# Kernel tuning notes

Hardware: AMD Instinct MI355X
Metric: run time of the kernel (lower is better)

Reference implementation:

```python
import jax, jax.numpy as jnp
import numpy as np

_INF = -1e30
EPS = 1e-8


def _masked_max(v, mask, axis, keepdims=False):
    return jnp.max(jnp.where(mask == 0, _INF, v), axis=axis, keepdims=keepdims)


def _masked_mean(v, mask, axis, keepdims=False):
    s = jnp.sum(jnp.where(mask == 0, 0.0, v), axis=axis, keepdims=keepdims)
    cnt = jnp.sum(jnp.broadcast_to(mask, v.shape), axis=axis, keepdims=keepdims)
    return s / jnp.clip(cnt, EPS, None)


def _masked_softmax(v, mask):
    return jax.nn.softmax(jnp.where(mask == 0, _INF, v), axis=-1)


def _cos(a, b, axis):
    num = jnp.sum(a * b, axis=axis)
    na = jnp.maximum(jnp.sqrt(jnp.sum(a * a, axis=axis)), EPS)
    nb = jnp.maximum(jnp.sqrt(jnp.sum(b * b, axis=axis)), EPS)
    return num / (na * nb)


def _pairwise_cos(c1, c2):
    # c1:[B,L1,H] c2:[B,L2,H] -> [B,L1,L2]
    dots = jnp.einsum('bih,bjh->bij', c1, c2)
    n1 = jnp.maximum(jnp.linalg.norm(c1, axis=-1), EPS)
    n2 = jnp.maximum(jnp.linalg.norm(c2, axis=-1), EPS)
    return dots / (n1[:, :, None] * n2[:, None, :])


def _mpm(v1, v2, w):
    # v1:[B,L,H], v2:[B,L or 1,H], w:[P,H]
    single = _cos(v1, v2, axis=2)[:, :, None]              # [B,L,1]
    wv1 = w[None, None] * v1[:, :, None, :]                # [B,L,P,H]
    wv2 = w[None, None] * v2[:, :, None, :]                # [B,Lv,P,H]
    multi = _cos(wv1, wv2, axis=3)                         # [B,L,P]
    return single, multi


def _mpm_pairwise(c1, c2, w):
    # w:[P,H] -> cosine [B,L1,L2,P]
    wv1 = w[None, :, None, :] * c1[:, None, :, :]          # [B,P,L1,H]
    wv2 = w[None, :, None, :] * c2[:, None, :, :]          # [B,P,L2,H]
    n1 = jnp.linalg.norm(wv1, axis=3, keepdims=True)       # [B,P,L1,1]
    n2 = jnp.linalg.norm(wv2, axis=3, keepdims=True)       # [B,P,L2,1]
    mul = jnp.einsum('bpih,bpjh->bpij', wv1, wv2)
    denom = jnp.clip(n1 * jnp.swapaxes(n2, 2, 3), EPS, None)
    return jnp.transpose(mul / denom, (0, 2, 3, 1))        # [B,L1,L2,P]


def _bimpm(context_1, mask_1, context_2, mask_2, w_ff, w_fb, w_mp, w_att, w_matt):
    B = context_1.shape[0]
    len1 = jnp.sum(mask_1, axis=1).astype(jnp.int32)
    len2 = jnp.sum(mask_2, axis=1).astype(jnp.int32)
    c1 = context_1 * mask_1[:, :, None]
    c2 = context_2 * mask_2[:, :, None]

    cos_sim = _pairwise_cos(c1, c2)                        # [B,L1,L2]
    m2r = mask_2[:, None, :]
    m1r = mask_1[:, None, :]
    cmax1 = _masked_max(cos_sim, m2r, 2, True)
    cmean1 = _masked_mean(cos_sim, m2r, 2, True)
    cos_t = jnp.swapaxes(cos_sim, 1, 2)
    cmax2 = _masked_max(cos_t, m1r, 2, True)
    cmean2 = _masked_mean(cos_t, m1r, 2, True)

    lp1 = jnp.clip(len1 - 1, 0, None)
    lp2 = jnp.clip(len2 - 1, 0, None)
    c1_fl = c1[jnp.arange(B), lp1][:, None, :]             # [B,1,H]
    c2_fl = c2[jnp.arange(B), lp2][:, None, :]
    c1_bl = c1[:, 0:1, :]
    c2_bl = c2[:, 0:1, :]

    mv1_ff = _mpm(c1, c2_fl, w_ff)
    mv2_ff = _mpm(c2, c1_fl, w_ff)
    mv1_bf = _mpm(c1, c2_bl, w_fb)
    mv2_bf = _mpm(c2, c1_bl, w_fb)

    mm = _mpm_pairwise(c1, c2, w_mp)                       # [B,L1,L2,P]
    mv1_max = _masked_max(mm, mask_2[:, None, :, None], 2)
    mv1_mean = _masked_mean(mm, mask_2[:, None, :, None], 2)
    mm_t = jnp.transpose(mm, (0, 2, 1, 3))
    mv2_max = _masked_max(mm_t, mask_1[:, None, :, None], 2)
    mv2_mean = _masked_mean(mm_t, mask_1[:, None, :, None], 2)

    att_2 = c2[:, None, :, :] * cos_sim[:, :, :, None]     # [B,L1,L2,H]
    att_1 = c1[:, :, None, :] * cos_sim[:, :, :, None]     # [B,L1,L2,H]
    att_mean_2 = _masked_softmax(att_2.sum(axis=2), mask_1[:, :, None])  # [B,L1,H]
    att_mean_1 = _masked_softmax(att_1.sum(axis=1), mask_2[:, :, None])  # [B,L2,H]
    mv1_am = _mpm(c1, att_mean_2, w_att)
    mv2_am = _mpm(c2, att_mean_1, w_att)

    att_max_2 = _masked_max(att_2, mask_2[:, None, :, None], 2)          # [B,L1,H]
    att_max_1 = _masked_max(jnp.transpose(att_1, (0, 2, 1, 3)), mask_1[:, None, :, None], 2)  # [B,L2,H]
    mv1_amx = _mpm(c1, att_max_2, w_matt)
    mv2_amx = _mpm(c2, att_max_1, w_matt)

    mv1 = jnp.concatenate([cmax1, cmean1, *mv1_ff, *mv1_bf, mv1_max, mv1_mean, *mv1_am, *mv1_amx], axis=-1)
    mv2 = jnp.concatenate([cmax2, cmean2, *mv2_ff, *mv2_bf, mv2_max, mv2_mean, *mv2_am, *mv2_amx], axis=-1)
    return jnp.concatenate([mv1, mv2], axis=1)             # [B, L1+L2, 102]


def setup_inputs() -> dict:
    key = jax.random.key(0)
    B, L, H, P = 8, 128, 768, 16
    ks = jax.random.split(key, 8)
    context_1 = jax.random.normal(ks[0], (B, L, H), dtype=jnp.float32)
    context_2 = jax.random.normal(ks[1], (B, L, H), dtype=jnp.float32)
    len1 = jax.random.randint(ks[2], (B,), L // 2, L + 1)
    len2 = jax.random.randint(ks[3], (B,), L // 2, L + 1)
    ar = jnp.arange(L)
    mask_1 = (ar[None, :] < len1[:, None]).astype(jnp.float32)
    mask_2 = (ar[None, :] < len2[:, None]).astype(jnp.float32)
    scale = np.sqrt(2.0 / H).astype(np.float32)
    w_ff = jax.random.normal(ks[4], (P, H), dtype=jnp.float32) * scale
    w_fb = jax.random.normal(ks[5], (P, H), dtype=jnp.float32) * scale
    w_mp = jax.random.normal(ks[6], (P, H), dtype=jnp.float32) * scale
    kk = jax.random.split(ks[7], 2)
    w_att = jax.random.normal(kk[0], (P, H), dtype=jnp.float32) * scale
    w_matt = jax.random.normal(kk[1], (P, H), dtype=jnp.float32) * scale
    return {"context_1": context_1, "mask_1": mask_1, "context_2": context_2, "mask_2": mask_2,
            "w_ff": w_ff, "w_fb": w_fb, "w_mp": w_mp, "w_att": w_att, "w_matt": w_matt}


def reference(context_1, mask_1, context_2, mask_2, w_ff, w_fb, w_mp, w_att, w_matt):
    return _bimpm(context_1, mask_1, context_2, mask_2, w_ff, w_fb, w_mp, w_att, w_matt)
```

## Files before the change

### kernel.cpp

```cpp
#include <hip/hip_runtime.h>

#define Bn 8
#define Ln 128
#define Hn 768
#define Pn 16
#define Dn 102
#define EPSF 1e-8f
#define NINF -1e30f

typedef __attribute__((ext_vector_type(8))) short bfrag8;
typedef __attribute__((ext_vector_type(4))) float f32x4;
union FragU { unsigned u[4]; bfrag8 v; };

#define MFMA16(A,B,C) __builtin_amdgcn_mfma_f32_16x16x32_bf16((A),(B),(C),0,0,0)

__device__ __forceinline__ float wred_sum(float v){
#pragma unroll
  for(int o=32;o>=1;o>>=1) v += __shfl_xor(v,o);
  return v;
}
__device__ __forceinline__ float wred_max(float v){
#pragma unroll
  for(int o=32;o>=1;o>>=1) v = fmaxf(v,__shfl_xor(v,o));
  return v;
}
__device__ __forceinline__ float qred_sum(float v){
  v += __shfl_xor(v,16);
  v += __shfl_xor(v,32);
  return v;
}

__device__ __forceinline__ void split8(const float* x, FragU& H, FragU& L){
  float r[8];
#pragma unroll
  for(int q=0;q<8;q++){
    unsigned hb = __float_as_uint(x[q]) & 0xffff0000u;
    r[q] = x[q] - __uint_as_float(hb);
  }
#pragma unroll
  for(int q=0;q<4;q++){
    H.u[q] = __builtin_amdgcn_perm(__float_as_uint(x[2*q+1]), __float_as_uint(x[2*q]), 0x07060302u);
    L.u[q] = __builtin_amdgcn_perm(__float_as_uint(r[2*q+1]), __float_as_uint(r[2*q]), 0x07060302u);
  }
}

#define GLD_LDS(gp, lp) __builtin_amdgcn_global_load_lds( \
    (const __attribute__((address_space(1))) void*)(gp), \
    (__attribute__((address_space(3))) void*)(lp), 16, 0, 0)

constexpr size_t SZ_MAT   = (size_t)Bn*Ln*Hn;
constexpr size_t OFF_C1F  = 0;
constexpr size_t OFF_C2F  = OFF_C1F + SZ_MAT;
constexpr size_t OFF_COS  = OFF_C2F + SZ_MAT;
constexpr size_t OFF_N1   = OFF_COS + (size_t)Bn*Ln*Ln;
constexpr size_t OFF_N2   = OFF_N1 + (size_t)Bn*Ln;
constexpr size_t OFF_WN   = OFF_N2 + (size_t)Bn*Ln;
constexpr size_t OFF_W2T  = OFF_WN + (size_t)2*5*Bn*Pn*Ln;
constexpr size_t OFF_MVMAX  = OFF_W2T + (size_t)5*Hn*Pn;
constexpr size_t OFF_MVMEAN = OFF_MVMAX + (size_t)2*Bn*Ln*Pn;
constexpr size_t OFF_PART   = OFF_MVMEAN + (size_t)2*Bn*Ln*Pn;
constexpr size_t OFF_LENS   = OFF_PART + (size_t)Bn*Ln*Pn*32*2;
constexpr size_t OFF_C2H    = OFF_LENS + 32;
constexpr size_t OFF_C2L    = OFF_C2H + (size_t)Bn*12*128*64/2;
constexpr size_t OFF_W2F    = OFF_C2L + (size_t)Bn*12*128*64/2;
constexpr size_t OFF_W2B    = OFF_W2F + 12288;

__device__ __forceinline__ size_t wnIdx(int side,int X,int b,int p,int i){
  return ((((size_t)side*5 + X)*Bn + b)*Pn + p)*Ln + i;
}

__global__ __launch_bounds__(256) void k_prep(
    const float* __restrict__ m1, const float* __restrict__ m2,
    const float* __restrict__ wff, const float* __restrict__ wfb,
    const float* __restrict__ wmp, const float* __restrict__ watt,
    const float* __restrict__ wmatt,
    float* __restrict__ W2T, float* __restrict__ W2F, float* __restrict__ W2B,
    int* __restrict__ lens){
  int t = threadIdx.x;
  const float* srcs[5] = {wff,wfb,wmp,watt,wmatt};
  if(blockIdx.x < 8){
    int b = blockIdx.x;
    __shared__ int cnt[2];
    if(t<2) cnt[t]=0;
    __syncthreads();
    if(t<Ln){
      if(m1[b*Ln+t]>0.5f) atomicAdd(&cnt[0],1);
      if(m2[b*Ln+t]>0.5f) atomicAdd(&cnt[1],1);
    }
    __syncthreads();
    if(t==0){
      lens[b]=cnt[0]; lens[8+b]=cnt[1];
      lens[16+b]=max(cnt[0]-1,0); lens[24+b]=max(cnt[1]-1,0);
    }
  } else if(blockIdx.x < 248){
    int idx = (blockIdx.x-8)*256 + t;
    int X = idx/(Pn*Hn);
    int r = idx%(Pn*Hn);
    int h = r/Pn, p = r%Pn;
    float w = srcs[X][p*Hn+h];
    W2T[idx] = w*w;
  } else if(blockIdx.x < 296){
    int idx = (blockIdx.x-248)*256 + t;
    int ksg = idx>>9;
    int r   = idx&511;
    int half= r>>8;
    int li  = (r>>2)&63;
    int e4  = r&3;
    int h = ksg*32 + half*16 + ((li>>4)<<2) + e4;
    int p = li&15;
    float w = wmp[p*Hn+h];
    W2F[idx] = w*w;
  } else {
    int idx = (blockIdx.x-296)*256 + t;
    int X   = idx/12288;
    int r   = idx%12288;
    int hh4 = r>>8;
    int li  = (r>>2)&63;
    int e   = r&3;
    int h = (li>>4)*192 + hh4*4 + e;
    int p = li&15;
    float w = srcs[X][p*Hn+h];
    W2B[idx] = w*w;
  }
}

__global__ __launch_bounds__(256) void k_rows(
    const float* __restrict__ ctx1, const float* __restrict__ m1,
    const float* __restrict__ ctx2, const float* __restrict__ m2,
    const float* __restrict__ W2T,
    float* __restrict__ c1f, float* __restrict__ c2f,
    unsigned short* __restrict__ c2h, unsigned short* __restrict__ c2l,
    float* __restrict__ n1, float* __restrict__ n2, float* __restrict__ wn){
  const int i0 = blockIdx.x*4, b = blockIdx.y, side = blockIdx.z;
  const float* ctx = side? ctx2 : ctx1;
  const float* msk = side? m2 : m1;
  float* dst = side? c2f : c1f;
  float* nD  = side? n2 : n1;
  const int t = threadIdx.x, w = t>>6, l = t&63;

  __shared__ float red4[4][4];
  __shared__ float redX[4][4][16];
  __shared__ float mkS[4];

  if(t<4) mkS[t] = msk[b*Ln+i0+t];

#pragma unroll
  for(int r=0;r<4;r++){
    const int i = i0+r;
    const float mk = msk[b*Ln+i];
    const size_t base = ((size_t)(b*Ln+i))*Hn;
    float ss = 0.f;
#pragma unroll
    for(int k=0;k<3;k++){
      float x = ctx[base + t + 256*k]*mk;
      dst[base + t + 256*k] = x;
      ss = fmaf(x,x,ss);
      if(side==1){
        int h = t+256*k;
        int kc = h>>6, hw = h&63, u = hw>>2, e = hw&3;
        int pos = ((u ^ (i&15))<<2) + e;
        size_t o = ((size_t)(b*12+kc)*128 + i)*64 + pos;
        unsigned hb = __float_as_uint(x) & 0xffff0000u;
        float rem = x - __uint_as_float(hb);
        c2h[o] = (unsigned short)(hb>>16);
        c2l[o] = (unsigned short)(__float_as_uint(rem)>>16);
      }
    }
    ss = wred_sum(ss);
    if(l==0) red4[r][w]=ss;
  }
  __syncthreads();
  if(t<4) nD[b*Ln+i0+t] = sqrtf(fmaxf(red4[t][0]+red4[t][1]+red4[t][2]+red4[t][3],0.f));

  const int pq = t&3, hc = t>>2;
  const int h0 = hc*12;
  float v2r[4][12];
#pragma unroll
  for(int r=0;r<4;r++){
    const float mk = mkS[r];
    const float* src = ctx + ((size_t)(b*Ln+i0+r))*Hn + h0;
#pragma unroll
    for(int q=0;q<3;q++){
      float4 xv = *(const float4*)(src + q*4);
      v2r[r][q*4+0]=xv.x*xv.x*mk; v2r[r][q*4+1]=xv.y*xv.y*mk;
      v2r[r][q*4+2]=xv.z*xv.z*mk; v2r[r][q*4+3]=xv.w*xv.w*mk;
    }
  }
  for(int X=0;X<5;++X){
    float acc[4][4];
#pragma unroll
    for(int r=0;r<4;r++){ acc[r][0]=0.f; acc[r][1]=0.f; acc[r][2]=0.f; acc[r][3]=0.f; }
    const float* wb = W2T + (size_t)X*Hn*Pn + pq*4;
#pragma unroll
    for(int h=0;h<12;h++){
      float4 w4 = *(const float4*)(wb + (size_t)(h0+h)*Pn);
#pragma unroll
      for(int r=0;r<4;r++){
        acc[r][0]=fmaf(w4.x,v2r[r][h],acc[r][0]);
        acc[r][1]=fmaf(w4.y,v2r[r][h],acc[r][1]);
        acc[r][2]=fmaf(w4.z,v2r[r][h],acc[r][2]);
        acc[r][3]=fmaf(w4.w,v2r[r][h],acc[r][3]);
      }
    }
#pragma unroll
    for(int r=0;r<4;r++)
#pragma unroll
      for(int pi=0;pi<4;pi++){
        float v = acc[r][pi];
        v += __shfl_xor(v,4); v += __shfl_xor(v,8);
        v += __shfl_xor(v,16); v += __shfl_xor(v,32);
        acc[r][pi]=v;
      }
    if(l<4){
#pragma unroll
      for(int r=0;r<4;r++)
#pragma unroll
        for(int pi=0;pi<4;pi++) redX[w][l][r*4+pi]=acc[r][pi];
    }
    __syncthreads();
    if(t<64){
      int r = t>>4, p = t&15;
      int pqi = p>>2, pii = p&3;
      float s = redX[0][pqi][r*4+pii]+redX[1][pqi][r*4+pii]
               +redX[2][pqi][r*4+pii]+redX[3][pqi][r*4+pii];
      wn[wnIdx(side,X,b,p,i0+r)] = s;
    }
    __syncthreads();
  }
}

__global__ __launch_bounds__(512) void k_mm(
    const float* __restrict__ c1f,
    const unsigned short* __restrict__ c2h, const unsigned short* __restrict__ c2l,
    const float* __restrict__ W2F, const float* __restrict__ WN,
    const float* __restrict__ n1, const float* __restrict__ n2,
    const float* __restrict__ m1, const float* __restrict__ m2,
    const int* __restrict__ lens,
    float* __restrict__ cosM,
    float* __restrict__ mvmax, float* __restrict__ mvmean,
    float* __restrict__ part){
  const int b = blockIdx.x, ig = blockIdx.y, ibase = ig*4;
  const int t = threadIdx.x, l = t&63;
  const int wid = __builtin_amdgcn_readfirstlane(t>>6);
  const int jtp = wid&3, ihalf = wid>>2;
  const int p = l&15, g4 = l>>4;

  __shared__ __align__(16) unsigned short sB2h[2][128][64];
  __shared__ __align__(16) unsigned short sB2l[2][128][64];
  __shared__ __align__(16) float sw2[2][1024];
  __shared__ __align__(16) float sa[2][4][64];
  __shared__ float sm2s[Ln];
  __shared__ float red0[2][4][2][16][2];

  const size_t c2elem = (size_t)b*12*8192;

  {
#pragma unroll
    for(int k=0;k<2;k++){
      GLD_LDS((const char*)c2h + c2elem*2 + (2*wid+k)*1024 + l*16,
              (char*)&sB2h[0][0][0] + (2*wid+k)*1024);
      GLD_LDS((const char*)c2l + c2elem*2 + (2*wid+k)*1024 + l*16,
              (char*)&sB2l[0][0][0] + (2*wid+k)*1024);
    }
    if(wid>=4){
      int q = wid-4;
      GLD_LDS((const char*)W2F + q*1024 + l*16,
              (char*)&sw2[0][0] + q*1024);
    }
    if(t<Ln) sm2s[t] = m2[b*Ln+t];
    if(t<64){
      int row = t>>4, u = t&15;
      float4 av = *(const float4*)(c1f + ((size_t)(b*Ln+ibase+row))*Hn + u*4);
      *(float4*)&sa[0][row][(u ^ (row&3))<<2] = av;
    }
  }
  __syncthreads();

  f32x4 accE[2][2]; f32x4 accC[2];
#pragma unroll
  for(int q=0;q<2;q++){
    accC[q] = (f32x4){0.f,0.f,0.f,0.f};
#pragma unroll
    for(int ii=0;ii<2;ii++) accE[q][ii] = (f32x4){0.f,0.f,0.f,0.f};
  }

  for(int c=0; c<12; ++c){
    const int cur = c&1, nxt = cur^1;
    const bool more = (c+1<12);
    float4 aN;
    if(more){
      const size_t cb2 = (c2elem + (size_t)(c+1)*8192)*2;
#pragma unroll
      for(int k=0;k<2;k++){
        GLD_LDS((const char*)c2h + cb2 + (2*wid+k)*1024 + l*16,
                (char*)&sB2h[nxt][0][0] + (2*wid+k)*1024);
        GLD_LDS((const char*)c2l + cb2 + (2*wid+k)*1024 + l*16,
                (char*)&sB2l[nxt][0][0] + (2*wid+k)*1024);
      }
      if(wid>=4){
        int q = wid-4;
        GLD_LDS((const char*)W2F + (c+1)*4096 + q*1024 + l*16,
                (char*)&sw2[nxt][0] + q*1024);
      }
      if(t<64){
        int row = t>>4, u = t&15;
        aN = *(const float4*)(c1f + ((size_t)(b*Ln+ibase+row))*Hn + (c+1)*64 + u*4);
      }
    }
#pragma unroll
    for(int ks=0; ks<2; ++ks){
      f32x4 w20 = *(const f32x4*)&sw2[cur][(ks*2+0)*256 + (l<<2)];
      f32x4 w21 = *(const f32x4*)&sw2[cur][(ks*2+1)*256 + (l<<2)];
      FragU Bh[2], Bl[2];
#pragma unroll
      for(int q=0;q<2;q++){
        int jt = jtp + 4*q;
        int j  = jt*16 + p;
        const char* bh = (const char*)&sB2h[cur][0][0] + j*128;
        const char* bl = (const char*)&sB2l[cur][0][0] + j*128;
        int u1 = (ks*8 + g4)     ^ (j&15);
        int u2 = (ks*8 + 4 + g4) ^ (j&15);
        uint2 h0 = *(const uint2*)(bh + (u1<<3));
        uint2 h1 = *(const uint2*)(bh + (u2<<3));
        uint2 l0 = *(const uint2*)(bl + (u1<<3));
        uint2 l1 = *(const uint2*)(bl + (u2<<3));
        Bh[q].u[0]=h0.x; Bh[q].u[1]=h0.y; Bh[q].u[2]=h1.x; Bh[q].u[3]=h1.y;
        Bl[q].u[0]=l0.x; Bl[q].u[1]=l0.y; Bl[q].u[2]=l1.x; Bl[q].u[3]=l1.y;
      }
      if(ihalf==0){
        int ar = p&3;
        const float* sar = &sa[cur][ar][0];
        f32x4 a0 = *(const f32x4*)(sar + (((ks*8+g4)  ^ar)<<2));
        f32x4 a1 = *(const f32x4*)(sar + (((ks*8+4+g4)^ar)<<2));
        float xv[8] = {a0[0],a0[1],a0[2],a0[3], a1[0],a1[1],a1[2],a1[3]};
        FragU Ah, Al; split8(xv, Ah, Al);
#pragma unroll
        for(int q=0;q<2;q++){
          accC[q] = MFMA16(Bh[q].v, Ah.v, accC[q]);
          accC[q] = MFMA16(Bh[q].v, Al.v, accC[q]);
          accC[q] = MFMA16(Bl[q].v, Ah.v, accC[q]);
        }
      }
#pragma unroll
      for(int ii=0;ii<2;ii++){
        int row = ihalf*2+ii;
        const float* sar = &sa[cur][row][0];
        f32x4 a0 = *(const f32x4*)(sar + (((ks*8+g4)  ^(row&3))<<2));
        f32x4 a1 = *(const f32x4*)(sar + (((ks*8+4+g4)^(row&3))<<2));
        float xv[8] = {a0[0]*w20[0], a0[1]*w20[1], a0[2]*w20[2], a0[3]*w20[3],
                       a1[0]*w21[0], a1[1]*w21[1], a1[2]*w21[2], a1[3]*w21[3]};
        FragU Ah, Al; split8(xv, Ah, Al);
#pragma unroll
        for(int q=0;q<2;q++){
          accE[q][ii] = MFMA16(Bh[q].v, Ah.v, accE[q][ii]);
          accE[q][ii] = MFMA16(Bh[q].v, Al.v, accE[q][ii]);
          accE[q][ii] = MFMA16(Bl[q].v, Ah.v, accE[q][ii]);
        }
      }
    }
    if(more && t<64){
      int row = t>>4, u = t&15;
      *(float4*)&sa[nxt][row][(u ^ (row&3))<<2] = aN;
    }
    __syncthreads();
  }

  const int len2 = min(max(lens[8+b],1),Ln);
  float sq1[2][4];
#pragma unroll
  for(int q=0;q<2;q++){
    int jt = jtp+4*q;
#pragma unroll
    for(int r=0;r<4;r++){
      int j = jt*16 + g4*4 + r;
      sq1[q][r] = sqrtf(fmaxf(WN[wnIdx(1,2,b,p,j)],0.f));
    }
  }
  float s1M[2][4], s1S[2][4];
#pragma unroll
  for(int q=0;q<2;q++)
#pragma unroll
    for(int r=0;r<4;r++){ s1M[q][r]=NINF; s1S[q][r]=0.f; }

#pragma unroll
  for(int ii=0;ii<2;ii++){
    int iR = ibase + ihalf*2 + ii;
    float sr = sqrtf(fmaxf(WN[wnIdx(0,2,b,p,iR)],0.f));
    float mr = m1[b*Ln+iR];
    float vmax=NINF, vsum=0.f;
#pragma unroll
    for(int q=0;q<2;q++){
      int jt = jtp+4*q;
#pragma unroll
      for(int r=0;r<4;r++){
        int j = jt*16 + g4*4 + r;
        float ev = accE[q][ii][r] / fmaxf(sr*sq1[q][r], EPSF);
        if(sm2s[j]!=0.f){ vmax=fmaxf(vmax,ev); vsum+=ev; }
        if(mr!=0.f){ s1M[q][r]=fmaxf(s1M[q][r],ev); s1S[q][r]+=ev; }
      }
    }
    vmax = fmaxf(vmax, __shfl_xor(vmax,16)); vmax = fmaxf(vmax, __shfl_xor(vmax,32));
    vsum += __shfl_xor(vsum,16); vsum += __shfl_xor(vsum,32);
    if(l<16){ red0[ihalf][jtp][ii][l][0]=vmax; red0[ihalf][jtp][ii][l][1]=vsum; }
  }
  float* red1 = (float*)&sB2h[0][0][0];
  if(ihalf==1){
#pragma unroll
    for(int q=0;q<2;q++)
#pragma unroll
      for(int r=0;r<4;r++){
        int idx = (((jtp*2+q)*64 + l)*4 + r)*2;
        red1[idx]   = s1M[q][r];
        red1[idx+1] = s1S[q][r];
      }
  }
  __syncthreads();
  if(t<64){
    int ih_=t>>5, ii_=(t>>4)&1, p_=t&15;
    float M=NINF,S=0.f;
#pragma unroll
    for(int jq=0;jq<4;jq++){ M=fmaxf(M,red0[ih_][jq][ii_][p_][0]); S+=red0[ih_][jq][ii_][p_][1]; }
    int iR = ibase + ih_*2 + ii_;
    size_t o = ((size_t)(b*Ln+iR))*Pn + p_;
    mvmax[o]=M; mvmean[o]=S/(float)len2;
  }
  if(ihalf==0){
#pragma unroll
    for(int q=0;q<2;q++){
      int jt = jtp+4*q;
#pragma unroll
      for(int r=0;r<4;r++){
        int j = jt*16 + g4*4 + r;
        int idx = (((jtp*2+q)*64 + l)*4 + r)*2;
        float M = fmaxf(s1M[q][r], red1[idx]);
        float S = s1S[q][r] + red1[idx+1];
        size_t o = ((((size_t)(b*Ln+j))*Pn + p)*32 + ig)*2;
        part[o]=M; part[o+1]=S;
        float nj = fmaxf(n2[b*Ln+j], EPSF);
        if(p<4){
          int iR = ibase + p;
          float ni = fmaxf(n1[b*Ln+iR], EPSF);
          cosM[((size_t)(b*Ln+iR))*Ln + j] = accC[q][r]/(ni*nj);
        }
      }
    }
  }
}

__global__ __launch_bounds__(256) void k_mm2(
    const float* __restrict__ part, const int* __restrict__ lens,
    float* __restrict__ mvmax, float* __restrict__ mvmean){
  int g = blockIdx.x*256 + threadIdx.x;
  int b = g>>11;
  const float4* q = (const float4*)(part + (size_t)g*64);
  float mx = NINF, sm = 0.f;
#pragma unroll
  for(int k=0;k<16;k++){
    float4 v = q[k];
    mx = fmaxf(mx, fmaxf(v.x, v.z));
    sm += v.y + v.w;
  }
  int len1 = min(max(lens[b],1),Ln);
  size_t o = (size_t)Bn*Ln*Pn + g;
  mvmax[o] = mx;
  mvmean[o] = sm/(float)len1;
}

#define HPAD 784
__global__ __launch_bounds__(256) void k_fin(
    const float* __restrict__ c1f, const float* __restrict__ c2f,
    const float* __restrict__ cosM,
    const float* __restrict__ n1, const float* __restrict__ n2,
    const float* __restrict__ wn, const float* __restrict__ W2B,
    const float* __restrict__ mvmax, const float* __restrict__ mvmean,
    const int* __restrict__ lens,
    const float* __restrict__ m1, const float* __restrict__ m2,
    float* __restrict__ out){
  const int x = blockIdx.x, side = x>>3, b = x&7;
  const int r0 = blockIdx.y*4;
  const int t = threadIdx.x, w = t>>6, l = t&63;
  const float* selfF  = side? c2f : c1f;
  const float* otherF = side? c1f : c2f;
  const float* nSelf  = side? n2 : n1;
  const float* nOther = side? n1 : n2;
  const float* mInner = side? m1 : m2;
  const float* mSelfm = side? m2 : m1;
  int lenI = side? lens[b]    : lens[8+b];
  int lpO  = side? lens[16+b] : lens[24+b];
  lenI = min(max(lenI,1),Ln);
  lpO  = min(max(lpO,0),Ln-1);

  __shared__ float cS[4*Ln];
  __shared__ float mS[Ln];
  __shared__ __align__(16) float sV1[4][HPAD];
  __shared__ __align__(16) float sF[HPAD], sB[HPAD];
  __shared__ __align__(16) float sAS[4][HPAD], sAM[4][HPAD];
  __shared__ float redm[4][4], reds[4][4];

  {
    if(side==0){
      const float* crow = cosM + ((size_t)(b*Ln+r0))*Ln;
      for(int idx=t; idx<4*Ln; idx+=256) cS[idx]=crow[idx];
    } else {
      for(int idx=t; idx<4*Ln; idx+=256){
        int jj = idx&127, rp = idx>>7;
        cS[rp*Ln+jj] = cosM[((size_t)(b*Ln+jj))*Ln + r0+rp];
      }
    }
    if(t<Ln) mS[t]=mInner[b*Ln+t];
    const float4* s4 = (const float4*)(selfF + ((size_t)(b*Ln+r0))*Hn);
    for(int idx=t; idx<4*Hn/4; idx+=256){
      int row = idx/192, q = idx - row*192;
      ((float4*)&sV1[row][0])[q + q/48] = s4[idx];
    }
    const float4* f4 = (const float4*)(otherF + ((size_t)(b*Ln+lpO))*Hn);
    const float4* b4 = (const float4*)(otherF + ((size_t)(b*Ln))*Hn);
    if(t<Hn/4){
      ((float4*)sF)[t + t/48]=f4[t];
      ((float4*)sB)[t + t/48]=b4[t];
    }
  }
  __syncthreads();

  float aS[4][3], aM[4][3];
#pragma unroll
  for(int r=0;r<4;r++)
#pragma unroll
    for(int k=0;k<3;k++){ aS[r][k]=0.f; aM[r][k]=NINF; }
  {
    const float* src = otherF + (size_t)b*Ln*Hn;
#pragma unroll 4
    for(int jj=0; jj<lenI; ++jj){
      float3 vk = ((const float3*)(src + (size_t)jj*Hn))[t];
      float c0=cS[jj], c1v=cS[Ln+jj], c2v=cS[2*Ln+jj], c3v=cS[3*Ln+jj];
      aS[0][0]=fmaf(vk.x,c0 ,aS[0][0]); aS[0][1]=fmaf(vk.y,c0 ,aS[0][1]); aS[0][2]=fmaf(vk.z,c0 ,aS[0][2]);
      aS[1][0]=fmaf(vk.x,c1v,aS[1][0]); aS[1][1]=fmaf(vk.y,c1v,aS[1][1]); aS[1][2]=fmaf(vk.z,c1v,aS[1][2]);
      aS[2][0]=fmaf(vk.x,c2v,aS[2][0]); aS[2][1]=fmaf(vk.y,c2v,aS[2][1]); aS[2][2]=fmaf(vk.z,c2v,aS[2][2]);
      aS[3][0]=fmaf(vk.x,c3v,aS[3][0]); aS[3][1]=fmaf(vk.y,c3v,aS[3][1]); aS[3][2]=fmaf(vk.z,c3v,aS[3][2]);
      aM[0][0]=fmaxf(aM[0][0],vk.x*c0 ); aM[0][1]=fmaxf(aM[0][1],vk.y*c0 ); aM[0][2]=fmaxf(aM[0][2],vk.z*c0 );
      aM[1][0]=fmaxf(aM[1][0],vk.x*c1v); aM[1][1]=fmaxf(aM[1][1],vk.y*c1v); aM[1][2]=fmaxf(aM[1][2],vk.z*c1v);
      aM[2][0]=fmaxf(aM[2][0],vk.x*c2v); aM[2][1]=fmaxf(aM[2][1],vk.y*c2v); aM[2][2]=fmaxf(aM[2][2],vk.z*c2v);
      aM[3][0]=fmaxf(aM[3][0],vk.x*c3v); aM[3][1]=fmaxf(aM[3][1],vk.y*c3v); aM[3][2]=fmaxf(aM[3][2],vk.z*c3v);
    }
  }

  {
#pragma unroll
    for(int r=0;r<4;r++){
      float lm = fmaxf(fmaxf(aS[r][0],aS[r][1]),aS[r][2]);
      lm = wred_max(lm);
      if(l==0) redm[r][w]=lm;
    }
  }
  __syncthreads();
  float bm[4];
#pragma unroll
  for(int r=0;r<4;r++)
    bm[r] = fmaxf(fmaxf(redm[r][0],redm[r][1]),fmaxf(redm[r][2],redm[r][3]));
  float ev[4][3];
  {
#pragma unroll
    for(int r=0;r<4;r++){
      float es=0.f;
#pragma unroll
      for(int k=0;k<3;k++){ ev[r][k]=expf(aS[r][k]-bm[r]); es+=ev[r][k]; }
      es = wred_sum(es);
      if(l==0) reds[r][w]=es;
    }
  }
  __syncthreads();
  {
    const float u = 1.f/(float)Hn;
#pragma unroll
    for(int r=0;r<4;r++){
      float smr = mSelfm[b*Ln+r0+r];
      float bs = reds[r][0]+reds[r][1]+reds[r][2]+reds[r][3];
      float inv = 1.f/fmaxf(bs,EPSF);
#pragma unroll
      for(int k=0;k<3;k++){
        int h = 3*t+k;
        int hi = h + ((h/192)<<2);
        sAS[r][hi] = (smr!=0.f)? ev[r][k]*inv : u;
        sAM[r][hi] = aM[r][k];
      }
    }
  }
  __syncthreads();

  {
    int rr = w;
    float cmx=NINF, csm=0.f;
    float ca = cS[rr*Ln + l], cb = cS[rr*Ln + l + 64];
    if(mS[l]!=0.f){ cmx=ca; csm=ca; }
    if(mS[l+64]!=0.f){ cmx=fmaxf(cmx,cb); csm+=cb; }
    cmx = wred_max(cmx); csm = wred_sum(csm);
    if(l==0){
      float* op = out + ((size_t)((b*2+side)*Ln + r0+rr))*Dn;
      op[0] = cmx;
      op[1] = csm/(float)lenI;
    }
  }
  if(t<128){
    int rr = t>>5, qq = t&31, p = qq&15;
    size_t o = ((size_t)((side*Bn+b)*Ln + r0+rr))*Pn + p;
    float* op = out + ((size_t)((b*2+side)*Ln + r0+rr))*Dn;
    if(qq<16) op[36+p] = mvmax[o];
    else      op[52+p] = mvmean[o];
  }

  {
    const int Xids[4] = {0,1,3,4};
    const int offS[4] = {2,19,68,85};
    const int X = Xids[w], offs = offS[w];
    const bool dyn = (w>=2);
    const int p = l&15, hq = l>>4;
    const int hb = hq*196;
    const float4* wB = (const float4*)W2B + (size_t)X*3072 + l;
    float acc[4]={0,0,0,0}, s0[4]={0,0,0,0};
    float sna[4]={0,0,0,0}, sn[4]={0,0,0,0};
    if(!dyn){
      const float* bvp = (w==0)? sF : sB;
#pragma unroll 4
      for(int h4=0; h4<48; ++h4){
        float4 w4 = wB[h4*64];
        float4 bv = *(const float4*)(bvp + hb + h4*4);
#pragma unroll
        for(int r=0;r<4;r++){
          float4 v = *(const float4*)(&sV1[r][hb + h4*4]);
          float pr;
          pr=v.x*bv.x; acc[r]=fmaf(w4.x,pr,acc[r]); s0[r]+=pr;
          pr=v.y*bv.y; acc[r]=fmaf(w4.y,pr,acc[r]); s0[r]+=pr;
          pr=v.z*bv.z; acc[r]=fmaf(w4.z,pr,acc[r]); s0[r]+=pr;
          pr=v.w*bv.w; acc[r]=fmaf(w4.w,pr,acc[r]); s0[r]+=pr;
        }
      }
    } else {
      const float (*bvp)[HPAD] = (w==2)? sAS : sAM;
#pragma unroll 2
      for(int h4=0; h4<48; ++h4){
        float4 w4 = wB[h4*64];
#pragma unroll
        for(int r=0;r<4;r++){
          float4 bv = *(const float4*)(&bvp[r][hb + h4*4]);
          float4 v  = *(const float4*)(&sV1[r][hb + h4*4]);
          float pr, bb;
          pr=v.x*bv.x; bb=bv.x*bv.x;
          acc[r]=fmaf(w4.x,pr,acc[r]); sna[r]=fmaf(w4.x,bb,sna[r]); s0[r]+=pr; sn[r]+=bb;
          pr=v.y*bv.y; bb=bv.y*bv.y;
          acc[r]=fmaf(w4.y,pr,acc[r]); sna[r]=fmaf(w4.y,bb,sna[r]); s0[r]+=pr; sn[r]+=bb;
          pr=v.z*bv.z; bb=bv.z*bv.z;
          acc[r]=fmaf(w4.z,pr,acc[r]); sna[r]=fmaf(w4.z,bb,sna[r]); s0[r]+=pr; sn[r]+=bb;
          pr=v.w*bv.w; bb=bv.w*bv.w;
          acc[r]=fmaf(w4.w,pr,acc[r]); sna[r]=fmaf(w4.w,bb,sna[r]); s0[r]+=pr; sn[r]+=bb;
        }
      }
    }
#pragma unroll
    for(int r=0;r<4;r++){
      acc[r]=qred_sum(acc[r]); s0[r]=qred_sum(s0[r]);
      if(dyn){ sna[r]=qred_sum(sna[r]); sn[r]=qred_sum(sn[r]); }
    }
#pragma unroll
    for(int rr=0; rr<4; ++rr){
      const int r = r0+rr;
      float* op = out + ((size_t)((b*2+side)*Ln + r))*Dn;
      if(l<16){
        float wa = fmaxf(wn[wnIdx(side,X,b,l,r)],0.f);
        float wb = dyn? fmaxf(sna[rr],0.f)
                      : fmaxf(wn[wnIdx(1-side,X,b,l,(w==0? lpO:0))],0.f);
        float mul = acc[rr]/(fmaxf(sqrtf(wa),EPSF)*fmaxf(sqrtf(wb),EPSF));
        op[offs+1+l] = mul;
      }
      if(l==0){
        float nb = dyn? sqrtf(fmaxf(sn[rr],0.f)) : nOther[b*Ln + (w==0? lpO : 0)];
        float nv1 = nSelf[b*Ln+r];
        op[offs] = s0[rr]/(fmaxf(nv1,EPSF)*fmaxf(nb,EPSF));
      }
    }
  }
}

extern "C" void kernel_launch(void* const* d_in, const int* in_sizes, int n_in,
                              void* d_out, int out_size, void* d_ws, size_t ws_size,
                              hipStream_t stream) {
  const float* ctx1 = (const float*)d_in[0];
  const float* m1   = (const float*)d_in[1];
  const float* ctx2 = (const float*)d_in[2];
  const float* m2   = (const float*)d_in[3];
  const float* wff  = (const float*)d_in[4];
  const float* wfb  = (const float*)d_in[5];
  const float* wmp  = (const float*)d_in[6];
  const float* watt = (const float*)d_in[7];
  const float* wmatt= (const float*)d_in[8];
  float* out = (float*)d_out;
  float* W = (float*)d_ws;
  int* lens = (int*)(W + OFF_LENS);
  unsigned short* c2h = (unsigned short*)(W + OFF_C2H);
  unsigned short* c2l = (unsigned short*)(W + OFF_C2L);

  k_prep<<<dim3(8 + 240 + 48 + 240), 256, 0, stream>>>(m1,m2,wff,wfb,wmp,watt,wmatt,
      W+OFF_W2T, W+OFF_W2F, W+OFF_W2B, lens);
  k_rows<<<dim3(Ln/4,Bn,2), 256, 0, stream>>>(ctx1,m1,ctx2,m2, W+OFF_W2T,
      W+OFF_C1F, W+OFF_C2F, c2h, c2l, W+OFF_N1, W+OFF_N2, W+OFF_WN);
  k_mm<<<dim3(Bn, 32), 512, 0, stream>>>(W+OFF_C1F, c2h, c2l,
      W+OFF_W2F, W+OFF_WN, W+OFF_N1, W+OFF_N2, m1, m2, lens,
      W+OFF_COS, W+OFF_MVMAX, W+OFF_MVMEAN, W+OFF_PART);
  k_mm2<<<dim3((Bn*Ln*Pn)/256), 256, 0, stream>>>(W+OFF_PART, lens,
      W+OFF_MVMAX, W+OFF_MVMEAN);
  k_fin<<<dim3(16, Ln/4), 256, 0, stream>>>(W+OFF_C1F, W+OFF_C2F, W+OFF_COS,
      W+OFF_N1, W+OFF_N2, W+OFF_WN, W+OFF_W2B, W+OFF_MVMAX, W+OFF_MVMEAN,
      lens, m1, m2, out);
}
```

Measured before the change: 161.4 us.

## Double-buffer other-side context rows into LDS with async global-to-LDS loads

```diff
diff --git a/kernel.cpp b/kernel.cpp
--- a/kernel.cpp
+++ b/kernel.cpp
@@ -479,6 +479,7 @@
   const int x = blockIdx.x, side = x>>3, b = x&7;
   const int r0 = blockIdx.y*4;
   const int t = threadIdx.x, w = t>>6, l = t&63;
+  const int wid = __builtin_amdgcn_readfirstlane(w);
   const float* selfF  = side? c2f : c1f;
   const float* otherF = side? c1f : c2f;
   const float* nSelf  = side? n2 : n1;
@@ -495,9 +496,19 @@
   __shared__ __align__(16) float sV1[4][HPAD];
   __shared__ __align__(16) float sF[HPAD], sB[HPAD];
   __shared__ __align__(16) float sAS[4][HPAD], sAM[4][HPAD];
+  __shared__ __align__(16) float sRow[2][4*Hn];
   __shared__ float redm[4][4], reds[4][4];
 
+  const float* panel = otherF + (size_t)b*Ln*Hn;
+
   {
+#pragma unroll
+    for(int k=0;k<3;k++){
+      int idx = k*256 + t;
+      int row = idx/192, q = idx - row*192;
+      GLD_LDS(panel + (size_t)row*Hn + q*4,
+              (char*)&sRow[0][0] + (k*256 + wid*64)*16);
+    }
     if(side==0){
       const float* crow = cosM + ((size_t)(b*Ln+r0))*Ln;
       for(int idx=t; idx<4*Ln; idx+=256) cS[idx]=crow[idx];
@@ -528,19 +539,39 @@
 #pragma unroll
     for(int k=0;k<3;k++){ aS[r][k]=0.f; aM[r][k]=NINF; }
   {
-    const float* src = otherF + (size_t)b*Ln*Hn;
-#pragma unroll 4
-    for(int jj=0; jj<lenI; ++jj){
-      float3 vk = ((const float3*)(src + (size_t)jj*Hn))[t];
-      float c0=cS[jj], c1v=cS[Ln+jj], c2v=cS[2*Ln+jj], c3v=cS[3*Ln+jj];
-      aS[0][0]=fmaf(vk.x,c0 ,aS[0][0]); aS[0][1]=fmaf(vk.y,c0 ,aS[0][1]); aS[0][2]=fmaf(vk.z,c0 ,aS[0][2]);
-      aS[1][0]=fmaf(vk.x,c1v,aS[1][0]); aS[1][1]=fmaf(vk.y,c1v,aS[1][1]); aS[1][2]=fmaf(vk.z,c1v,aS[1][2]);
-      aS[2][0]=fmaf(vk.x,c2v,aS[2][0]); aS[2][1]=fmaf(vk.y,c2v,aS[2][1]); aS[2][2]=fmaf(vk.z,c2v,aS[2][2]);
-      aS[3][0]=fmaf(vk.x,c3v,aS[3][0]); aS[3][1]=fmaf(vk.y,c3v,aS[3][1]); aS[3][2]=fmaf(vk.z,c3v,aS[3][2]);
-      aM[0][0]=fmaxf(aM[0][0],vk.x*c0 ); aM[0][1]=fmaxf(aM[0][1],vk.y*c0 ); aM[0][2]=fmaxf(aM[0][2],vk.z*c0 );
-      aM[1][0]=fmaxf(aM[1][0],vk.x*c1v); aM[1][1]=fmaxf(aM[1][1],vk.y*c1v); aM[1][2]=fmaxf(aM[1][2],vk.z*c1v);
-      aM[2][0]=fmaxf(aM[2][0],vk.x*c2v); aM[2][1]=fmaxf(aM[2][1],vk.y*c2v); aM[2][2]=fmaxf(aM[2][2],vk.z*c2v);
-      aM[3][0]=fmaxf(aM[3][0],vk.x*c3v); aM[3][1]=fmaxf(aM[3][1],vk.y*c3v); aM[3][2]=fmaxf(aM[3][2],vk.z*c3v);
+    const int nch = (lenI+3)>>2;
+    for(int c=0; c<nch; ++c){
+      const int cur = c&1;
+      if(c+1<nch){
+        const int nxt = cur^1;
+        const float* gsrc = panel + (size_t)(c+1)*4*Hn;
+#pragma unroll
+        for(int k=0;k<3;k++){
+          int idx = k*256 + t;
+          int row = idx/192, q = idx - row*192;
+          GLD_LDS(gsrc + (size_t)row*Hn + q*4,
+                  (char*)&sRow[nxt][0] + (k*256 + wid*64)*16);
+        }
+      }
+      const float* rb = &sRow[cur][0] + 3*t;
+      const int jc = c*4;
+#pragma unroll
+      for(int k4=0;k4<4;k4++){
+        int jj = jc + k4;
+        if(jj >= lenI) break;
+        const float* rp = rb + k4*Hn;
+        float vx = rp[0], vy = rp[1], vz = rp[2];
+        float c0=cS[jj], c1v=cS[Ln+jj], c2v=cS[2*Ln+jj], c3v=cS[3*Ln+jj];
+        aS[0][0]=fmaf(vx,c0 ,aS[0][0]); aS[0][1]=fmaf(vy,c0 ,aS[0][1]); aS[0][2]=fmaf(vz,c0 ,aS[0][2]);
+        aS[1][0]=fmaf(vx,c1v,aS[1][0]); aS[1][1]=fmaf(vy,c1v,aS[1][1]); aS[1][2]=fmaf(vz,c1v,aS[1][2]);
+        aS[2][0]=fmaf(vx,c2v,aS[2][0]); aS[2][1]=fmaf(vy,c2v,aS[2][1]); aS[2][2]=fmaf(vz,c2v,aS[2][2]);
+        aS[3][0]=fmaf(vx,c3v,aS[3][0]); aS[3][1]=fmaf(vy,c3v,aS[3][1]); aS[3][2]=fmaf(vz,c3v,aS[3][2]);
+        aM[0][0]=fmaxf(aM[0][0],vx*c0 ); aM[0][1]=fmaxf(aM[0][1],vy*c0 ); aM[0][2]=fmaxf(aM[0][2],vz*c0 );
+        aM[1][0]=fmaxf(aM[1][0],vx*c1v); aM[1][1]=fmaxf(aM[1][1],vy*c1v); aM[1][2]=fmaxf(aM[1][2],vz*c1v);
+        aM[2][0]=fmaxf(aM[2][0],vx*c2v); aM[2][1]=fmaxf(aM[2][1],vy*c2v); aM[2][2]=fmaxf(aM[2][2],vz*c2v);
+        aM[3][0]=fmaxf(aM[3][0],vx*c3v); aM[3][1]=fmaxf(aM[3][1],vy*c3v); aM[3][2]=fmaxf(aM[3][2],vz*c3v);
+      }
+      __syncthreads();
     }
   }
 
```

Result: slower. 176.0 us (+9.0%).
